# Performance work log

Measured on AMD Instinct MI355X. Metric: run time of the kernel, lower is better.

## Reference

```python
import jax, jax.numpy as jnp
import numpy as np

L, B, F, D = 12, 2048, 6144, 768

def setup_inputs() -> dict:
    key = jax.random.key(0)
    k1, k2, k3 = jax.random.split(key, 3)
    acts = jax.random.normal(k1, (L, B, F), dtype=jnp.float32)
    # decoder weights for target layer: stacked per source layer, [L, F, D]
    W = jax.random.normal(k2, (L, F, D), dtype=jnp.float32) * 0.02
    bias = jax.random.normal(k3, (L, D), dtype=jnp.float32) * 0.01
    return {"acts": acts, "W": W, "bias": bias, "layer_idx": 11}

def reference(acts, W, bias, layer_idx):
    # decode(): sum over src_layer <= layer_idx of Linear(a[src], W[src->tgt], b[src->tgt])
    n = layer_idx + 1  # static Python int -> static slice
    a = acts[:n]       # [n, B, F]
    w = W[:n]          # [n, F, D]
    b = bias[:n]       # [n, D]
    # fused accumulation of all per-source-layer GEMMs
    recon = jnp.einsum('lbf,lfd->bd', a, w) + jnp.sum(b, axis=0)  # [B, D]
    return recon
```

## Files before the change

### kernel.cpp

```cpp
#include <hip/hip_runtime.h>
#include <hip/hip_bf16.h>

#define NB 2048
#define NF 6144
#define ND 768
#define BM 256
#define BN 192
#define BK 64
#define SPLITK 2
#define KCH (NF / SPLITK)
#define NTIL (KCH / BK)

#define ABYTES (BM * 128)
#define BBYTES (BN * 128)
#define BUFBYTES (ABYTES + BBYTES)

typedef __attribute__((ext_vector_type(8))) __bf16 bf16x8;
typedef __attribute__((ext_vector_type(4))) float f32x4;

__device__ __forceinline__ char* lds_addr(char* base, int row, int k) {
  const int blk = ((k >> 3) ^ (row & 7) ^ ((row >> 2) & 7)) & 7;
  return base + row * 128 + (blk << 4) + ((k & 7) << 1);
}

#define BAR()                                              \
  do {                                                     \
    asm volatile("s_waitcnt lgkmcnt(0)" ::: "memory");     \
    __builtin_amdgcn_sched_barrier(0);                     \
    __builtin_amdgcn_s_barrier();                          \
    __builtin_amdgcn_sched_barrier(0);                     \
  } while (0)

__global__ __launch_bounds__(256) void bias_init_kernel(
    const float* __restrict__ bias, const int* __restrict__ lidx,
    float* __restrict__ out) {
  int n = lidx[0] + 1;
  int i = blockIdx.x * 256 + threadIdx.x;
  if (i >= NB * ND) return;
  int d = i % ND;
  float s = 0.f;
  for (int l = 0; l < n; ++l) s += bias[l * ND + d];
  out[i] = s;
}

__global__ __launch_bounds__(512, 2) void gemm_kernel(
    const float* __restrict__ acts, const float* __restrict__ W,
    const int* __restrict__ lidx, float* __restrict__ out, int nwg) {
  extern __shared__ char cbuf[];

  const int chunk = nwg >> 3;
  const int swz = (blockIdx.x & 7) * chunk + (blockIdx.x >> 3);
  const int by = swz & 3;
  int rem = swz >> 2;
  const int m = rem & 7; rem >>= 3;
  const int ks = rem & 1; rem >>= 1;
  const int l = rem;
  if (l > lidx[0]) return;

  const int brow = m * BM;
  const int ncol = by * BN;
  const int k0 = ks * KCH;

  const int tid = threadIdx.x;
  const int lane = tid & 63;
  const int wid = tid >> 6;
  const int wrow = (wid >> 1) * 64;
  const int wcol = (wid & 1) * 96;

  f32x4 acc[4][6];
#pragma unroll
  for (int i = 0; i < 4; ++i)
#pragma unroll
    for (int j = 0; j < 6; ++j) acc[i][j] = (f32x4){0.f, 0.f, 0.f, 0.f};

  const int s_arow = tid >> 3;
  const int s_ak = (tid & 7) * 8;
  const bool bstage = tid < 384;
  const int s_bd = (tid % 48) * 4;
  const int s_bk = (tid / 48) * 8;

  const float* Aptr =
      acts + (size_t)l * NB * NF + (size_t)(brow + s_arow) * NF + k0 + s_ak;
  const float* Bptr =
      W + (size_t)l * NF * ND + (size_t)(k0 + s_bk) * ND + (ncol + s_bd);

  float4 av[4][2];
  float4 bv[8];

  auto LOADS = [&](int kb) {
#pragma unroll
    for (int p = 0; p < 4; ++p) {
      av[p][0] = *(const float4*)(Aptr + (size_t)(64 * p) * NF + kb);
      av[p][1] = *(const float4*)(Aptr + (size_t)(64 * p) * NF + kb + 4);
    }
    if (bstage) {
#pragma unroll
      for (int j = 0; j < 8; ++j)
        bv[j] = *(const float4*)(Bptr + (size_t)(kb + j) * ND);
    }
  };

  auto STORE = [&](char* cA_, char* cB_) {
#pragma unroll
    for (int p = 0; p < 4; ++p) {
      bf16x8 h;
      h[0] = (__bf16)av[p][0].x; h[1] = (__bf16)av[p][0].y;
      h[2] = (__bf16)av[p][0].z; h[3] = (__bf16)av[p][0].w;
      h[4] = (__bf16)av[p][1].x; h[5] = (__bf16)av[p][1].y;
      h[6] = (__bf16)av[p][1].z; h[7] = (__bf16)av[p][1].w;
      *(bf16x8*)lds_addr(cA_, s_arow + 64 * p, s_ak) = h;
    }
    if (bstage) {
#pragma unroll
      for (int dd = 0; dd < 4; ++dd) {
        bf16x8 h;
#pragma unroll
        for (int j = 0; j < 8; ++j) h[j] = (__bf16)bv[j][dd];
        *(bf16x8*)lds_addr(cB_, s_bd + dd, s_bk) = h;
      }
    }
  };

  LOADS(0);
  STORE(cbuf, cbuf + ABYTES);

  for (int t = 0; t < NTIL; ++t) {
    BAR();
    const int cur = t & 1;
    char* rA = cbuf + (size_t)cur * BUFBYTES;
    char* rB = rA + ABYTES;
    char* wA = cbuf + (size_t)(cur ^ 1) * BUFBYTES;
    char* wB = wA + ABYTES;

    if (t + 1 < NTIL) LOADS((t + 1) * BK);
    __builtin_amdgcn_sched_barrier(0);

    bf16x8 aF[4][2];
#pragma unroll
    for (int mi = 0; mi < 4; ++mi)
#pragma unroll
      for (int s = 0; s < 2; ++s)
        aF[mi][s] = *(const bf16x8*)lds_addr(
            rA, wrow + mi * 16 + (lane & 15), s * 32 + (lane >> 4) * 8);

#pragma unroll
    for (int p = 0; p < 3; ++p) {
      bf16x8 bF[2][2];
#pragma unroll
      for (int ni = 0; ni < 2; ++ni)
#pragma unroll
        for (int s = 0; s < 2; ++s)
          bF[ni][s] = *(const bf16x8*)lds_addr(
              rB, wcol + (2 * p + ni) * 16 + (lane & 15),
              s * 32 + (lane >> 4) * 8);
      __builtin_amdgcn_s_setprio(1);
#pragma unroll
      for (int s = 0; s < 2; ++s)
#pragma unroll
        for (int mi = 0; mi < 4; ++mi)
#pragma unroll
          for (int ni = 0; ni < 2; ++ni)
            acc[mi][2 * p + ni] = __builtin_amdgcn_mfma_f32_16x16x32_bf16(
                aF[mi][s], bF[ni][s], acc[mi][2 * p + ni], 0, 0, 0);
      __builtin_amdgcn_s_setprio(0);
      __builtin_amdgcn_sched_barrier(0);
    }

    if (t + 1 < NTIL) STORE(wA, wB);
  }

  const int orow = brow + wrow + ((lane >> 4) << 2);
  const int ocol = ncol + wcol + (lane & 15);
#pragma unroll
  for (int mi = 0; mi < 4; ++mi)
#pragma unroll
    for (int ni = 0; ni < 6; ++ni)
#pragma unroll
      for (int j = 0; j < 4; ++j)
        atomicAdd(out + (size_t)(orow + mi * 16 + j) * ND + (ocol + ni * 16),
                  acc[mi][ni][j]);
}

extern "C" void kernel_launch(void* const* d_in, const int* in_sizes, int n_in,
                              void* d_out, int out_size, void* d_ws, size_t ws_size,
                              hipStream_t stream) {
  const float* acts = (const float*)d_in[0];
  const float* W    = (const float*)d_in[1];
  const float* bias = (const float*)d_in[2];
  const int*   lidx = (const int*)d_in[3];
  float* out = (float*)d_out;

  const int L = in_sizes[0] / (NB * NF);
  const int nwg = (ND / BN) * (NB / BM) * SPLITK * L;

  hipFuncSetAttribute((const void*)gemm_kernel,
                      hipFuncAttributeMaxDynamicSharedMemorySize,
                      2 * BUFBYTES);

  bias_init_kernel<<<dim3((NB * ND + 255) / 256), 256, 0, stream>>>(bias, lidx, out);
  gemm_kernel<<<dim3(nwg), 512, 2 * BUFBYTES, stream>>>(acts, W, lidx, out, nwg);
}
```

Baseline: 475.3 us.

## Interleave split A/B global loads and LDS stores across MFMA phases with barriers

Splits the next-tile global prefetch into separate A and B loads and the LDS write-back into separate A and B stores, then spreads them across the three MFMA sub-phases of each K tile. Each sub-phase gets its own workgroup barrier plus an LDS wait, ping-pong style, so memory traffic and compute are staggered rather than bunched at loop ends. The aim is better overlap of the load/convert/store path with MFMA work. The cost is extra barriers per iteration, which may add sync overhead and shift register pressure.

```diff
diff --git a/kernel.cpp b/kernel.cpp
--- a/kernel.cpp
+++ b/kernel.cpp
@@ -23,11 +23,9 @@
   return base + row * 128 + (blk << 4) + ((k & 7) << 1);
 }
 
-#define BAR()                                              \
+#define LGKM0()                                            \
   do {                                                     \
     asm volatile("s_waitcnt lgkmcnt(0)" ::: "memory");     \
-    __builtin_amdgcn_sched_barrier(0);                     \
-    __builtin_amdgcn_s_barrier();                          \
     __builtin_amdgcn_sched_barrier(0);                     \
   } while (0)
 
@@ -87,20 +85,21 @@
   float4 av[4][2];
   float4 bv[8];
 
-  auto LOADS = [&](int kb) {
+  auto ALOADS = [&](int kb) {
 #pragma unroll
     for (int p = 0; p < 4; ++p) {
       av[p][0] = *(const float4*)(Aptr + (size_t)(64 * p) * NF + kb);
       av[p][1] = *(const float4*)(Aptr + (size_t)(64 * p) * NF + kb + 4);
     }
+  };
+  auto BLOADS = [&](int kb) {
     if (bstage) {
 #pragma unroll
       for (int j = 0; j < 8; ++j)
         bv[j] = *(const float4*)(Bptr + (size_t)(kb + j) * ND);
     }
   };
-
-  auto STORE = [&](char* cA_, char* cB_) {
+  auto ASTORE = [&](char* cA_) {
 #pragma unroll
     for (int p = 0; p < 4; ++p) {
       bf16x8 h;
@@ -110,6 +109,8 @@
       h[6] = (__bf16)av[p][1].z; h[7] = (__bf16)av[p][1].w;
       *(bf16x8*)lds_addr(cA_, s_arow + 64 * p, s_ak) = h;
     }
+  };
+  auto BSTORE = [&](char* cB_) {
     if (bstage) {
 #pragma unroll
       for (int dd = 0; dd < 4; ++dd) {
@@ -121,20 +122,24 @@
     }
   };
 
-  LOADS(0);
-  STORE(cbuf, cbuf + ABYTES);
+  ALOADS(0);
+  BLOADS(0);
+  ASTORE(cbuf);
+  BSTORE(cbuf + ABYTES);
 
   for (int t = 0; t < NTIL; ++t) {
-    BAR();
     const int cur = t & 1;
     char* rA = cbuf + (size_t)cur * BUFBYTES;
     char* rB = rA + ABYTES;
     char* wA = cbuf + (size_t)(cur ^ 1) * BUFBYTES;
     char* wB = wA + ABYTES;
-
-    if (t + 1 < NTIL) LOADS((t + 1) * BK);
+    const bool more = (t + 1 < NTIL);
+
+    LGKM0();
+    __builtin_amdgcn_s_barrier();
     __builtin_amdgcn_sched_barrier(0);
 
+    if (more) ALOADS((t + 1) * BK);
     bf16x8 aF[4][2];
 #pragma unroll
     for (int mi = 0; mi < 4; ++mi)
@@ -142,17 +147,16 @@
       for (int s = 0; s < 2; ++s)
         aF[mi][s] = *(const bf16x8*)lds_addr(
             rA, wrow + mi * 16 + (lane & 15), s * 32 + (lane >> 4) * 8);
-
-#pragma unroll
-    for (int p = 0; p < 3; ++p) {
+    {
       bf16x8 bF[2][2];
 #pragma unroll
       for (int ni = 0; ni < 2; ++ni)
 #pragma unroll
         for (int s = 0; s < 2; ++s)
           bF[ni][s] = *(const bf16x8*)lds_addr(
-              rB, wcol + (2 * p + ni) * 16 + (lane & 15),
-              s * 32 + (lane >> 4) * 8);
+              rB, wcol + ni * 16 + (lane & 15), s * 32 + (lane >> 4) * 8);
+      __builtin_amdgcn_s_barrier();
+      LGKM0();
       __builtin_amdgcn_s_setprio(1);
 #pragma unroll
       for (int s = 0; s < 2; ++s)
@@ -160,13 +164,61 @@
         for (int mi = 0; mi < 4; ++mi)
 #pragma unroll
           for (int ni = 0; ni < 2; ++ni)
-            acc[mi][2 * p + ni] = __builtin_amdgcn_mfma_f32_16x16x32_bf16(
-                aF[mi][s], bF[ni][s], acc[mi][2 * p + ni], 0, 0, 0);
+            acc[mi][ni] = __builtin_amdgcn_mfma_f32_16x16x32_bf16(
+                aF[mi][s], bF[ni][s], acc[mi][ni], 0, 0, 0);
       __builtin_amdgcn_s_setprio(0);
       __builtin_amdgcn_sched_barrier(0);
     }
 
-    if (t + 1 < NTIL) STORE(wA, wB);
+    if (more) BLOADS((t + 1) * BK);
+    {
+      bf16x8 bF[2][2];
+#pragma unroll
+      for (int ni = 0; ni < 2; ++ni)
+#pragma unroll
+        for (int s = 0; s < 2; ++s)
+          bF[ni][s] = *(const bf16x8*)lds_addr(
+              rB, wcol + (2 + ni) * 16 + (lane & 15), s * 32 + (lane >> 4) * 8);
+      __builtin_amdgcn_s_barrier();
+      LGKM0();
+      __builtin_amdgcn_s_setprio(1);
+#pragma unroll
+      for (int s = 0; s < 2; ++s)
+#pragma unroll
+        for (int mi = 0; mi < 4; ++mi)
+#pragma unroll
+          for (int ni = 0; ni < 2; ++ni)
+            acc[mi][2 + ni] = __builtin_amdgcn_mfma_f32_16x16x32_bf16(
+                aF[mi][s], bF[ni][s], acc[mi][2 + ni], 0, 0, 0);
+      __builtin_amdgcn_s_setprio(0);
+      __builtin_amdgcn_sched_barrier(0);
+    }
+
+    if (more) ASTORE(wA);
+    {
+      bf16x8 bF[2][2];
+#pragma unroll
+      for (int ni = 0; ni < 2; ++ni)
+#pragma unroll
+        for (int s = 0; s < 2; ++s)
+          bF[ni][s] = *(const bf16x8*)lds_addr(
+              rB, wcol + (4 + ni) * 16 + (lane & 15), s * 32 + (lane >> 4) * 8);
+      __builtin_amdgcn_s_barrier();
+      LGKM0();
+      __builtin_amdgcn_s_setprio(1);
+#pragma unroll
+      for (int s = 0; s < 2; ++s)
+#pragma unroll
+        for (int mi = 0; mi < 4; ++mi)
+#pragma unroll
+          for (int ni = 0; ni < 2; ++ni)
+            acc[mi][4 + ni] = __builtin_amdgcn_mfma_f32_16x16x32_bf16(
+                aF[mi][s], bF[ni][s], acc[mi][4 + ni], 0, 0, 0);
+      __builtin_amdgcn_s_setprio(0);
+      __builtin_amdgcn_sched_barrier(0);
+    }
+
+    if (more) BSTORE(wB);
   }
 
   const int orow = brow + wrow + ((lane >> 4) << 2);
```

Result: slower. 499.3 us (+5.0%).

## Pre-convert activations to bf16 and stream A tiles via direct global-to-LDS loads

Applied to the files above, without the earlier changes.

Adds a separate pass that converts the fp32 activations to bf16 in the workspace. The GEMM then loads A tiles with asynchronous global_load_lds into the swizzled LDS layout, which removes the in-kernel fp32-to-bf16 conversion and A staging registers. Barriers become explicit vmcnt and lgkmcnt waits. The cost is an extra full read and write of activations in the conversion pass, and the old fused path is kept as a fallback when the workspace is too small.

```diff
diff --git a/kernel.cpp b/kernel.cpp
--- a/kernel.cpp
+++ b/kernel.cpp
@@ -18,18 +18,41 @@
 typedef __attribute__((ext_vector_type(8))) __bf16 bf16x8;
 typedef __attribute__((ext_vector_type(4))) float f32x4;
 
+__device__ __forceinline__ int swzf(int row) {
+  return ((row & 7) ^ ((row >> 2) & 7)) & 7;
+}
 __device__ __forceinline__ char* lds_addr(char* base, int row, int k) {
-  const int blk = ((k >> 3) ^ (row & 7) ^ ((row >> 2) & 7)) & 7;
+  const int blk = ((k >> 3) ^ swzf(row)) & 7;
   return base + row * 128 + (blk << 4) + ((k & 7) << 1);
 }
 
-#define BAR()                                              \
+__device__ __forceinline__ void async_ld16(void* lds, const void* g) {
+  __builtin_amdgcn_global_load_lds(
+      (const __attribute__((address_space(1))) void*)g,
+      (__attribute__((address_space(3))) void*)lds, 16, 0, 0);
+}
+
+#define LGKM0()                                            \
   do {                                                     \
     asm volatile("s_waitcnt lgkmcnt(0)" ::: "memory");     \
     __builtin_amdgcn_sched_barrier(0);                     \
-    __builtin_amdgcn_s_barrier();                          \
-    __builtin_amdgcn_sched_barrier(0);                     \
   } while (0)
+#define WAITVM(N) asm volatile("s_waitcnt vmcnt(" #N ")" ::: "memory")
+
+__global__ __launch_bounds__(256) void cvt_acts_kernel(
+    const float* __restrict__ acts, const int* __restrict__ lidx,
+    unsigned short* __restrict__ wsA) {
+  const size_t n8 = (size_t)(lidx[0] + 1) * NB * NF / 8;
+  const size_t stride = (size_t)gridDim.x * 256;
+  for (size_t i = (size_t)blockIdx.x * 256 + threadIdx.x; i < n8; i += stride) {
+    float4 a = ((const float4*)acts)[2 * i];
+    float4 b = ((const float4*)acts)[2 * i + 1];
+    bf16x8 h;
+    h[0] = (__bf16)a.x; h[1] = (__bf16)a.y; h[2] = (__bf16)a.z; h[3] = (__bf16)a.w;
+    h[4] = (__bf16)b.x; h[5] = (__bf16)b.y; h[6] = (__bf16)b.z; h[7] = (__bf16)b.w;
+    ((bf16x8*)wsA)[i] = h;
+  }
+}
 
 __global__ __launch_bounds__(256) void bias_init_kernel(
     const float* __restrict__ bias, const int* __restrict__ lidx,
@@ -43,8 +66,8 @@
   out[i] = s;
 }
 
-__global__ __launch_bounds__(512, 2) void gemm_kernel(
-    const float* __restrict__ acts, const float* __restrict__ W,
+__global__ __launch_bounds__(512, 2) void gemm_bf16a(
+    const unsigned short* __restrict__ actsb, const float* __restrict__ W,
     const int* __restrict__ lidx, float* __restrict__ out, int nwg) {
   extern __shared__ char cbuf[];
 
@@ -73,20 +96,144 @@
 #pragma unroll
     for (int j = 0; j < 6; ++j) acc[i][j] = (f32x4){0.f, 0.f, 0.f, 0.f};
 
-  const int s_arow = tid >> 3;
-  const int s_ak = (tid & 7) * 8;
+  const unsigned short* aSrc[4];
+  int ldsAoff[4];
+#pragma unroll
+  for (int j = 0; j < 4; ++j) {
+    const int r = 8 * wid + 64 * j + (lane >> 3);
+    const int kblk = (lane & 7) ^ swzf(r);
+    aSrc[j] = actsb + (size_t)l * NB * NF + (size_t)(brow + r) * NF + k0 + kblk * 8;
+    ldsAoff[j] = (8 * wid + 64 * j) * 128;
+  }
+
   const bool bstage = tid < 384;
   const int s_bd = (tid % 48) * 4;
   const int s_bk = (tid / 48) * 8;
-
+  const float* Bptr =
+      W + (size_t)l * NF * ND + (size_t)(k0 + s_bk) * ND + (ncol + s_bd);
+  float4 bv[8];
+
+  auto AGLOADS = [&](int kt, int buf) {
+    char* base = cbuf + (size_t)buf * BUFBYTES;
+#pragma unroll
+    for (int j = 0; j < 4; ++j)
+      async_ld16(base + ldsAoff[j], aSrc[j] + kt * BK);
+  };
+  auto BLOADS = [&](int kb) {
+    if (bstage) {
+#pragma unroll
+      for (int j = 0; j < 8; ++j)
+        bv[j] = *(const float4*)(Bptr + (size_t)(kb + j) * ND);
+    }
+  };
+  auto BSTORE = [&](int buf) {
+    if (bstage) {
+      char* cB_ = cbuf + (size_t)buf * BUFBYTES + ABYTES;
+#pragma unroll
+      for (int dd = 0; dd < 4; ++dd) {
+        bf16x8 h;
+#pragma unroll
+        for (int j = 0; j < 8; ++j) h[j] = (__bf16)bv[j][dd];
+        *(bf16x8*)lds_addr(cB_, s_bd + dd, s_bk) = h;
+      }
+    }
+  };
+
+  AGLOADS(0, 0);
+  BLOADS(0);
+  BSTORE(0);
+
+  for (int t = 0; t < NTIL; ++t) {
+    const int cur = t & 1;
+    char* rA = cbuf + (size_t)cur * BUFBYTES;
+    char* rB = rA + ABYTES;
+    const bool more = (t + 1 < NTIL);
+
+    if (more) {
+      AGLOADS(t + 1, cur ^ 1);
+      BLOADS((t + 1) * BK);
+      if (bstage) { WAITVM(12); } else { WAITVM(4); }
+    } else {
+      WAITVM(0);
+    }
+    LGKM0();
+    __builtin_amdgcn_s_barrier();
+    __builtin_amdgcn_sched_barrier(0);
+
+    bf16x8 aF[4][2];
+#pragma unroll
+    for (int mi = 0; mi < 4; ++mi)
+#pragma unroll
+      for (int s = 0; s < 2; ++s)
+        aF[mi][s] = *(const bf16x8*)lds_addr(
+            rA, wrow + mi * 16 + (lane & 15), s * 32 + (lane >> 4) * 8);
+#pragma unroll
+    for (int p = 0; p < 3; ++p) {
+      bf16x8 bF[2][2];
+#pragma unroll
+      for (int ni = 0; ni < 2; ++ni)
+#pragma unroll
+        for (int s = 0; s < 2; ++s)
+          bF[ni][s] = *(const bf16x8*)lds_addr(
+              rB, wcol + (2 * p + ni) * 16 + (lane & 15),
+              s * 32 + (lane >> 4) * 8);
+      LGKM0();
+      __builtin_amdgcn_s_setprio(1);
+#pragma unroll
+      for (int s = 0; s < 2; ++s)
+#pragma unroll
+        for (int mi = 0; mi < 4; ++mi)
+#pragma unroll
+          for (int ni = 0; ni < 2; ++ni)
+            acc[mi][2 * p + ni] = __builtin_amdgcn_mfma_f32_16x16x32_bf16(
+                aF[mi][s], bF[ni][s], acc[mi][2 * p + ni], 0, 0, 0);
+      __builtin_amdgcn_s_setprio(0);
+      __builtin_amdgcn_sched_barrier(0);
+    }
+
+    if (more) BSTORE(cur ^ 1);
+  }
+
+  const int orow = brow + wrow + ((lane >> 4) << 2);
+  const int ocol = ncol + wcol + (lane & 15);
+#pragma unroll
+  for (int mi = 0; mi < 4; ++mi)
+#pragma unroll
+    for (int ni = 0; ni < 6; ++ni)
+#pragma unroll
+      for (int j = 0; j < 4; ++j)
+        atomicAdd(out + (size_t)(orow + mi * 16 + j) * ND + (ocol + ni * 16),
+                  acc[mi][ni][j]);
+}
+
+__global__ __launch_bounds__(512, 2) void gemm_fused(
+    const float* __restrict__ acts, const float* __restrict__ W,
+    const int* __restrict__ lidx, float* __restrict__ out, int nwg) {
+  extern __shared__ char cbuf[];
+  const int chunk = nwg >> 3;
+  const int swz = (blockIdx.x & 7) * chunk + (blockIdx.x >> 3);
+  const int by = swz & 3;
+  int rem = swz >> 2;
+  const int m = rem & 7; rem >>= 3;
+  const int ks = rem & 1; rem >>= 1;
+  const int l = rem;
+  if (l > lidx[0]) return;
+  const int brow = m * BM, ncol = by * BN, k0 = ks * KCH;
+  const int tid = threadIdx.x, lane = tid & 63, wid = tid >> 6;
+  const int wrow = (wid >> 1) * 64, wcol = (wid & 1) * 96;
+  f32x4 acc[4][6];
+#pragma unroll
+  for (int i = 0; i < 4; ++i)
+#pragma unroll
+    for (int j = 0; j < 6; ++j) acc[i][j] = (f32x4){0.f, 0.f, 0.f, 0.f};
+  const int s_arow = tid >> 3, s_ak = (tid & 7) * 8;
+  const bool bstage = tid < 384;
+  const int s_bd = (tid % 48) * 4, s_bk = (tid / 48) * 8;
   const float* Aptr =
       acts + (size_t)l * NB * NF + (size_t)(brow + s_arow) * NF + k0 + s_ak;
   const float* Bptr =
       W + (size_t)l * NF * ND + (size_t)(k0 + s_bk) * ND + (ncol + s_bd);
-
-  float4 av[4][2];
-  float4 bv[8];
-
+  float4 av[4][2]; float4 bv[8];
   auto LOADS = [&](int kb) {
 #pragma unroll
     for (int p = 0; p < 4; ++p) {
@@ -99,7 +246,6 @@
         bv[j] = *(const float4*)(Bptr + (size_t)(kb + j) * ND);
     }
   };
-
   auto STORE = [&](char* cA_, char* cB_) {
 #pragma unroll
     for (int p = 0; p < 4; ++p) {
@@ -120,21 +266,19 @@
       }
     }
   };
-
   LOADS(0);
   STORE(cbuf, cbuf + ABYTES);
-
   for (int t = 0; t < NTIL; ++t) {
-    BAR();
     const int cur = t & 1;
     char* rA = cbuf + (size_t)cur * BUFBYTES;
     char* rB = rA + ABYTES;
     char* wA = cbuf + (size_t)(cur ^ 1) * BUFBYTES;
     char* wB = wA + ABYTES;
-
+    LGKM0();
+    __builtin_amdgcn_s_barrier();
+    __builtin_amdgcn_sched_barrier(0);
     if (t + 1 < NTIL) LOADS((t + 1) * BK);
     __builtin_amdgcn_sched_barrier(0);
-
     bf16x8 aF[4][2];
 #pragma unroll
     for (int mi = 0; mi < 4; ++mi)
@@ -142,7 +286,6 @@
       for (int s = 0; s < 2; ++s)
         aF[mi][s] = *(const bf16x8*)lds_addr(
             rA, wrow + mi * 16 + (lane & 15), s * 32 + (lane >> 4) * 8);
-
 #pragma unroll
     for (int p = 0; p < 3; ++p) {
       bf16x8 bF[2][2];
@@ -153,6 +296,7 @@
           bF[ni][s] = *(const bf16x8*)lds_addr(
               rB, wcol + (2 * p + ni) * 16 + (lane & 15),
               s * 32 + (lane >> 4) * 8);
+      LGKM0();
       __builtin_amdgcn_s_setprio(1);
 #pragma unroll
       for (int s = 0; s < 2; ++s)
@@ -165,10 +309,8 @@
       __builtin_amdgcn_s_setprio(0);
       __builtin_amdgcn_sched_barrier(0);
     }
-
     if (t + 1 < NTIL) STORE(wA, wB);
   }
-
   const int orow = brow + wrow + ((lane >> 4) << 2);
   const int ocol = ncol + wcol + (lane & 15);
 #pragma unroll
@@ -192,11 +334,19 @@
 
   const int L = in_sizes[0] / (NB * NF);
   const int nwg = (ND / BN) * (NB / BM) * SPLITK * L;
-
-  hipFuncSetAttribute((const void*)gemm_kernel,
-                      hipFuncAttributeMaxDynamicSharedMemorySize,
-                      2 * BUFBYTES);
+  const size_t wsNeed = (size_t)L * NB * NF * 2;
 
   bias_init_kernel<<<dim3((NB * ND + 255) / 256), 256, 0, stream>>>(bias, lidx, out);
-  gemm_kernel<<<dim3(nwg), 512, 2 * BUFBYTES, stream>>>(acts, W, lidx, out, nwg);
-}
+
+  if (ws_size >= wsNeed) {
+    unsigned short* wsA = (unsigned short*)d_ws;
+    cvt_acts_kernel<<<dim3(2048), 256, 0, stream>>>(acts, lidx, wsA);
+    hipFuncSetAttribute((const void*)gemm_bf16a,
+                        hipFuncAttributeMaxDynamicSharedMemorySize, 2 * BUFBYTES);
+    gemm_bf16a<<<dim3(nwg), 512, 2 * BUFBYTES, stream>>>(wsA, W, lidx, out, nwg);
+  } else {
+    hipFuncSetAttribute((const void*)gemm_fused,
+                        hipFuncAttributeMaxDynamicSharedMemorySize, 2 * BUFBYTES);
+    gemm_fused<<<dim3(nwg), 512, 2 * BUFBYTES, stream>>>(acts, W, lidx, out, nwg);
+  }
+}
```

Result: slower. 637.1 us (+34.0%).

## Pre-transpose W to bf16 workspace and stream B tiles via async global-to-LDS loads

Applied to the files above, without the earlier changes.

Adds a pre-pass kernel that transposes and converts W to bf16 in the workspace, laid out K-major with the LDS swizzle folded into the source addresses. The GEMM can then load B tiles with direct global_load_lds DMA instead of staging fp32 through registers. This cuts B register pressure, conversion work and global traffic for W inside the GEMM. In exchange it adds an extra kernel that reads all L layers of W and writes a bf16 copy every call, even layers that are skipped, plus a finer-grained waitcnt schedule. A fallback fused kernel is kept for when the workspace is too small.

```diff
diff --git a/kernel.cpp b/kernel.cpp
--- a/kernel.cpp
+++ b/kernel.cpp
@@ -13,22 +13,34 @@
 
 #define ABYTES (BM * 128)
 #define BBYTES (BN * 128)
-#define BUFBYTES (ABYTES + BBYTES)
-
+#define BUFB (ABYTES + BBYTES)
+
+typedef __attribute__((ext_vector_type(4))) __bf16 bf16x4;
 typedef __attribute__((ext_vector_type(8))) __bf16 bf16x8;
 typedef __attribute__((ext_vector_type(4))) float f32x4;
 
+__device__ __forceinline__ int fswz(int r) { return ((r & 7) ^ ((r >> 2) & 7)) & 7; }
 __device__ __forceinline__ char* lds_addr(char* base, int row, int k) {
-  const int blk = ((k >> 3) ^ (row & 7) ^ ((row >> 2) & 7)) & 7;
+  const int blk = ((k >> 3) ^ fswz(row)) & 7;
   return base + row * 128 + (blk << 4) + ((k & 7) << 1);
 }
 
-#define BAR()                                              \
-  do {                                                     \
-    asm volatile("s_waitcnt lgkmcnt(0)" ::: "memory");     \
-    __builtin_amdgcn_sched_barrier(0);                     \
-    __builtin_amdgcn_s_barrier();                          \
-    __builtin_amdgcn_sched_barrier(0);                     \
+__device__ __forceinline__ void async_ld16(void* lds, const void* g) {
+  __builtin_amdgcn_global_load_lds(
+      (const __attribute__((address_space(1))) void*)g,
+      (__attribute__((address_space(3))) void*)lds, 16, 0, 0);
+}
+
+#define SBAR0() __builtin_amdgcn_sched_barrier(0)
+#define LGKM(N)                                              \
+  do {                                                       \
+    asm volatile("s_waitcnt lgkmcnt(" #N ")" ::: "memory");  \
+    SBAR0();                                                 \
+  } while (0)
+#define VMW(N)                                               \
+  do {                                                       \
+    asm volatile("s_waitcnt vmcnt(" #N ")" ::: "memory");    \
+    SBAR0();                                                 \
   } while (0)
 
 __global__ __launch_bounds__(256) void bias_init_kernel(
@@ -43,8 +55,39 @@
   out[i] = s;
 }
 
-__global__ __launch_bounds__(512, 2) void gemm_kernel(
-    const float* __restrict__ acts, const float* __restrict__ W,
+__global__ __launch_bounds__(256) void wt_kernel(
+    const float* __restrict__ W, unsigned short* __restrict__ wt) {
+  __shared__ float t[64][65];
+  const int l = blockIdx.z, f0 = blockIdx.x * 64, d0 = blockIdx.y * 64;
+  const int tid = threadIdx.x;
+  const int fr = tid >> 4;
+  const int dc4 = (tid & 15) * 4;
+  const float* src = W + ((size_t)l * NF + f0 + fr) * ND + d0 + dc4;
+#pragma unroll
+  for (int i = 0; i < 4; ++i) {
+    float4 v = *(const float4*)(src + (size_t)16 * i * ND);
+    t[fr + 16 * i][dc4 + 0] = v.x;
+    t[fr + 16 * i][dc4 + 1] = v.y;
+    t[fr + 16 * i][dc4 + 2] = v.z;
+    t[fr + 16 * i][dc4 + 3] = v.w;
+  }
+  __syncthreads();
+  const int dr = tid >> 4;
+  const int fc4 = (tid & 15) * 4;
+  unsigned short* dst = wt + ((size_t)l * ND + d0 + dr) * NF + f0 + fc4;
+#pragma unroll
+  for (int i = 0; i < 4; ++i) {
+    bf16x4 h;
+    h[0] = (__bf16)t[fc4 + 0][dr + 16 * i];
+    h[1] = (__bf16)t[fc4 + 1][dr + 16 * i];
+    h[2] = (__bf16)t[fc4 + 2][dr + 16 * i];
+    h[3] = (__bf16)t[fc4 + 3][dr + 16 * i];
+    *(bf16x4*)(dst + (size_t)16 * i * NF) = h;
+  }
+}
+
+__global__ __launch_bounds__(512, 2) void gemm_dma(
+    const float* __restrict__ acts, const unsigned short* __restrict__ wt,
     const int* __restrict__ lidx, float* __restrict__ out, int nwg) {
   extern __shared__ char cbuf[];
 
@@ -75,32 +118,35 @@
 
   const int s_arow = tid >> 3;
   const int s_ak = (tid & 7) * 8;
-  const bool bstage = tid < 384;
-  const int s_bd = (tid % 48) * 4;
-  const int s_bk = (tid / 48) * 8;
-
   const float* Aptr =
       acts + (size_t)l * NB * NF + (size_t)(brow + s_arow) * NF + k0 + s_ak;
-  const float* Bptr =
-      W + (size_t)l * NF * ND + (size_t)(k0 + s_bk) * ND + (ncol + s_bd);
-
   float4 av[4][2];
-  float4 bv[8];
-
-  auto LOADS = [&](int kb) {
+
+  const unsigned short* bSrc[3];
+  int bDst[3];
+#pragma unroll
+  for (int j = 0; j < 3; ++j) {
+    const int r0 = 8 * (3 * wid + j);
+    const int r = r0 + (lane >> 3);
+    const int ksl = (lane & 7) ^ fswz(r);
+    bSrc[j] = wt + ((size_t)l * ND + ncol + r) * NF + k0 + ksl * 8;
+    bDst[j] = ABYTES + r0 * 128;
+  }
+
+  auto ALOADS = [&](int kb) {
 #pragma unroll
     for (int p = 0; p < 4; ++p) {
       av[p][0] = *(const float4*)(Aptr + (size_t)(64 * p) * NF + kb);
       av[p][1] = *(const float4*)(Aptr + (size_t)(64 * p) * NF + kb + 4);
     }
-    if (bstage) {
-#pragma unroll
-      for (int j = 0; j < 8; ++j)
-        bv[j] = *(const float4*)(Bptr + (size_t)(kb + j) * ND);
-    }
-  };
-
-  auto STORE = [&](char* cA_, char* cB_) {
+  };
+  auto DMA_B = [&](int t, int buf) {
+    char* b = cbuf + (size_t)buf * BUFB;
+#pragma unroll
+    for (int j = 0; j < 3; ++j)
+      async_ld16(b + bDst[j], bSrc[j] + (size_t)t * BK);
+  };
+  auto ASTORE = [&](char* cA_) {
 #pragma unroll
     for (int p = 0; p < 4; ++p) {
       bf16x8 h;
@@ -110,6 +156,139 @@
       h[6] = (__bf16)av[p][1].z; h[7] = (__bf16)av[p][1].w;
       *(bf16x8*)lds_addr(cA_, s_arow + 64 * p, s_ak) = h;
     }
+  };
+
+#define BF_READ(dst, P)                                                   \
+  _Pragma("unroll") for (int ni = 0; ni < 2; ++ni)                        \
+    _Pragma("unroll") for (int s = 0; s < 2; ++s)                         \
+      dst[ni][s] = *(const bf16x8*)lds_addr(                              \
+          rB, wcol + (2 * (P) + ni) * 16 + (lane & 15),                   \
+          s * 32 + (lane >> 4) * 8);
+
+#define MFMA16(bf, P)                                                     \
+  __builtin_amdgcn_s_setprio(1);                                          \
+  _Pragma("unroll") for (int s = 0; s < 2; ++s)                           \
+    _Pragma("unroll") for (int mi = 0; mi < 4; ++mi)                      \
+      _Pragma("unroll") for (int ni = 0; ni < 2; ++ni)                    \
+        acc[mi][2 * (P) + ni] = __builtin_amdgcn_mfma_f32_16x16x32_bf16(  \
+            aF[mi][s], bf[ni][s], acc[mi][2 * (P) + ni], 0, 0, 0);        \
+  __builtin_amdgcn_s_setprio(0);                                          \
+  SBAR0();
+
+  ALOADS(0);
+  DMA_B(0, 0);
+  ASTORE(cbuf);
+  VMW(0);
+  LGKM(0);
+
+  for (int t = 0; t < NTIL; ++t) {
+    const int cur = t & 1;
+    char* rA = cbuf + (size_t)cur * BUFB;
+    char* rB = rA + ABYTES;
+    char* wA = cbuf + (size_t)(cur ^ 1) * BUFB;
+    const bool more = (t + 1 < NTIL);
+
+    __builtin_amdgcn_s_barrier();
+    SBAR0();
+
+    if (more) {
+      ALOADS((t + 1) * BK);
+      DMA_B(t + 1, cur ^ 1);
+    }
+    SBAR0();
+
+    bf16x8 aF[4][2];
+#pragma unroll
+    for (int mi = 0; mi < 4; ++mi)
+#pragma unroll
+      for (int s = 0; s < 2; ++s)
+        aF[mi][s] = *(const bf16x8*)lds_addr(
+            rA, wrow + mi * 16 + (lane & 15), s * 32 + (lane >> 4) * 8);
+    bf16x8 bFa[2][2], bFb[2][2], bFc[2][2];
+    BF_READ(bFa, 0)
+    BF_READ(bFb, 1)
+    SBAR0();
+    LGKM(4);
+    MFMA16(bFa, 0)
+
+    BF_READ(bFc, 2)
+    SBAR0();
+    LGKM(4);
+    MFMA16(bFb, 1)
+
+    LGKM(0);
+    MFMA16(bFc, 2)
+
+    if (more) ASTORE(wA);
+    VMW(0);
+    LGKM(0);
+  }
+
+#undef BF_READ
+#undef MFMA16
+
+  const int orow = brow + wrow + ((lane >> 4) << 2);
+  const int ocol = ncol + wcol + (lane & 15);
+#pragma unroll
+  for (int mi = 0; mi < 4; ++mi)
+#pragma unroll
+    for (int ni = 0; ni < 6; ++ni)
+#pragma unroll
+      for (int j = 0; j < 4; ++j)
+        atomicAdd(out + (size_t)(orow + mi * 16 + j) * ND + (ocol + ni * 16),
+                  acc[mi][ni][j]);
+}
+
+__global__ __launch_bounds__(512, 2) void gemm_fused(
+    const float* __restrict__ acts, const float* __restrict__ W,
+    const int* __restrict__ lidx, float* __restrict__ out, int nwg) {
+  extern __shared__ char cbuf[];
+  const int chunk = nwg >> 3;
+  const int swz = (blockIdx.x & 7) * chunk + (blockIdx.x >> 3);
+  const int by = swz & 3;
+  int rem = swz >> 2;
+  const int m = rem & 7; rem >>= 3;
+  const int ks = rem & 1; rem >>= 1;
+  const int l = rem;
+  if (l > lidx[0]) return;
+  const int brow = m * BM, ncol = by * BN, k0 = ks * KCH;
+  const int tid = threadIdx.x, lane = tid & 63, wid = tid >> 6;
+  const int wrow = (wid >> 1) * 64, wcol = (wid & 1) * 96;
+  f32x4 acc[4][6];
+#pragma unroll
+  for (int i = 0; i < 4; ++i)
+#pragma unroll
+    for (int j = 0; j < 6; ++j) acc[i][j] = (f32x4){0.f, 0.f, 0.f, 0.f};
+  const int s_arow = tid >> 3, s_ak = (tid & 7) * 8;
+  const bool bstage = tid < 384;
+  const int s_bd = (tid % 48) * 4, s_bk = (tid / 48) * 8;
+  const float* Aptr =
+      acts + (size_t)l * NB * NF + (size_t)(brow + s_arow) * NF + k0 + s_ak;
+  const float* Bptr =
+      W + (size_t)l * NF * ND + (size_t)(k0 + s_bk) * ND + (ncol + s_bd);
+  float4 av[4][2]; float4 bv[8];
+  auto LOADS = [&](int kb) {
+#pragma unroll
+    for (int p = 0; p < 4; ++p) {
+      av[p][0] = *(const float4*)(Aptr + (size_t)(64 * p) * NF + kb);
+      av[p][1] = *(const float4*)(Aptr + (size_t)(64 * p) * NF + kb + 4);
+    }
+    if (bstage) {
+#pragma unroll
+      for (int j = 0; j < 8; ++j)
+        bv[j] = *(const float4*)(Bptr + (size_t)(kb + j) * ND);
+    }
+  };
+  auto STORE = [&](char* cA_, char* cB_) {
+#pragma unroll
+    for (int p = 0; p < 4; ++p) {
+      bf16x8 h;
+      h[0] = (__bf16)av[p][0].x; h[1] = (__bf16)av[p][0].y;
+      h[2] = (__bf16)av[p][0].z; h[3] = (__bf16)av[p][0].w;
+      h[4] = (__bf16)av[p][1].x; h[5] = (__bf16)av[p][1].y;
+      h[6] = (__bf16)av[p][1].z; h[7] = (__bf16)av[p][1].w;
+      *(bf16x8*)lds_addr(cA_, s_arow + 64 * p, s_ak) = h;
+    }
     if (bstage) {
 #pragma unroll
       for (int dd = 0; dd < 4; ++dd) {
@@ -120,21 +299,19 @@
       }
     }
   };
-
   LOADS(0);
   STORE(cbuf, cbuf + ABYTES);
-
   for (int t = 0; t < NTIL; ++t) {
-    BAR();
     const int cur = t & 1;
-    char* rA = cbuf + (size_t)cur * BUFBYTES;
+    char* rA = cbuf + (size_t)cur * BUFB;
     char* rB = rA + ABYTES;
-    char* wA = cbuf + (size_t)(cur ^ 1) * BUFBYTES;
+    char* wA = cbuf + (size_t)(cur ^ 1) * BUFB;
     char* wB = wA + ABYTES;
-
+    LGKM(0);
+    __builtin_amdgcn_s_barrier();
+    SBAR0();
     if (t + 1 < NTIL) LOADS((t + 1) * BK);
-    __builtin_amdgcn_sched_barrier(0);
-
+    SBAR0();
     bf16x8 aF[4][2];
 #pragma unroll
     for (int mi = 0; mi < 4; ++mi)
@@ -142,7 +319,6 @@
       for (int s = 0; s < 2; ++s)
         aF[mi][s] = *(const bf16x8*)lds_addr(
             rA, wrow + mi * 16 + (lane & 15), s * 32 + (lane >> 4) * 8);
-
 #pragma unroll
     for (int p = 0; p < 3; ++p) {
       bf16x8 bF[2][2];
@@ -153,6 +329,7 @@
           bF[ni][s] = *(const bf16x8*)lds_addr(
               rB, wcol + (2 * p + ni) * 16 + (lane & 15),
               s * 32 + (lane >> 4) * 8);
+      LGKM(0);
       __builtin_amdgcn_s_setprio(1);
 #pragma unroll
       for (int s = 0; s < 2; ++s)
@@ -163,12 +340,10 @@
             acc[mi][2 * p + ni] = __builtin_amdgcn_mfma_f32_16x16x32_bf16(
                 aF[mi][s], bF[ni][s], acc[mi][2 * p + ni], 0, 0, 0);
       __builtin_amdgcn_s_setprio(0);
-      __builtin_amdgcn_sched_barrier(0);
-    }
-
+      SBAR0();
+    }
     if (t + 1 < NTIL) STORE(wA, wB);
   }
-
   const int orow = brow + wrow + ((lane >> 4) << 2);
   const int ocol = ncol + wcol + (lane & 15);
 #pragma unroll
@@ -192,11 +367,19 @@
 
   const int L = in_sizes[0] / (NB * NF);
   const int nwg = (ND / BN) * (NB / BM) * SPLITK * L;
-
-  hipFuncSetAttribute((const void*)gemm_kernel,
-                      hipFuncAttributeMaxDynamicSharedMemorySize,
-                      2 * BUFBYTES);
+  const size_t wsNeed = (size_t)L * NF * ND * 2;
 
   bias_init_kernel<<<dim3((NB * ND + 255) / 256), 256, 0, stream>>>(bias, lidx, out);
-  gemm_kernel<<<dim3(nwg), 512, 2 * BUFBYTES, stream>>>(acts, W, lidx, out, nwg);
-}
+
+  if (ws_size >= wsNeed) {
+    unsigned short* wsB = (unsigned short*)d_ws;
+    wt_kernel<<<dim3(NF / 64, ND / 64, L), 256, 0, stream>>>(W, wsB);
+    hipFuncSetAttribute((const void*)gemm_dma,
+                        hipFuncAttributeMaxDynamicSharedMemorySize, 2 * BUFB);
+    gemm_dma<<<dim3(nwg), 512, 2 * BUFB, stream>>>(acts, wsB, lidx, out, nwg);
+  } else {
+    hipFuncSetAttribute((const void*)gemm_fused,
+                        hipFuncAttributeMaxDynamicSharedMemorySize, 2 * BUFB);
+    gemm_fused<<<dim3(nwg), 512, 2 * BUFB, stream>>>(acts, W, lidx, out, nwg);
+  }
+}
```

Result: slower. 542.7 us (+14.2%).
